# Performance work log

Hardware: AMD Instinct MI355X
Metric: run time of the kernel (lower is better)

Reference implementation:

```python
import jax, jax.numpy as jnp
import numpy as np

D = 512
SEG_LEN = 128
RCL = 32          # right_context_length
K = 31            # depthwise kernel size
STATE = K - 1     # state_size = 30
U = 2048          # utterance length = 16 segments * SEG_LEN
R = 512           # right context length total = 16 * RCL
B = 32
EPS = 1e-5


def layer_norm(x, g, b):
    m = jnp.mean(x, axis=-1, keepdims=True)
    v = jnp.mean((x - m) ** 2, axis=-1, keepdims=True)
    return (x - m) * jax.lax.rsqrt(v + EPS) * g + b


def dwconv(x, w, b):
    # x: [N, D, T], w: [D, 1, K] depthwise, b: [D]
    y = jax.lax.conv_general_dilated(
        x, w, window_strides=(1,), padding='VALID',
        dimension_numbers=('NCH', 'OIH', 'NCH'), feature_group_count=x.shape[1])
    return y + b[None, :, None]


def setup_inputs() -> dict:
    key = jax.random.key(0)
    ks = jax.random.split(key, 8)
    s = 0.02
    return {
        'utterance': jax.random.normal(ks[0], (U, B, D), jnp.float32),
        'right_context': jax.random.normal(ks[1], (R, B, D), jnp.float32),
        'state': jnp.zeros((B, D, STATE), jnp.float32),
        'ln1_g': jnp.ones((D,), jnp.float32),
        'ln1_b': jnp.zeros((D,), jnp.float32),
        'w1': jax.random.normal(ks[2], (2 * D, D), jnp.float32) * s,
        'b1': jnp.zeros((2 * D,), jnp.float32),
        'conv_w': jax.random.normal(ks[3], (D, 1, K), jnp.float32) * s,
        'conv_b': jnp.zeros((D,), jnp.float32),
        'ln2_g': jnp.ones((D,), jnp.float32),
        'ln2_b': jnp.zeros((D,), jnp.float32),
        'w2': jax.random.normal(ks[4], (D, D), jnp.float32) * s,
        'b2': jnp.zeros((D,), jnp.float32),
    }


def reference(utterance, right_context, state, ln1_g, ln1_b, w1, b1,
              conv_w, conv_b, ln2_g, ln2_b, w2, b2):
    inp = jnp.concatenate((right_context, utterance), axis=0)  # [R+U, B, D]
    # pre_conv: LayerNorm -> Linear(D, 2D) -> GLU
    x = layer_norm(inp, ln1_g, ln1_b) @ w1.T + b1
    a, g = jnp.split(x, 2, axis=-1)
    x = a * jax.nn.sigmoid(g)                                  # [R+U, B, D]
    x_rc, x_utt = x[:R], x[R:]
    x_utt_t = jnp.transpose(x_utt, (1, 2, 0))                  # [B, D, U]
    state_x = jnp.concatenate([state, x_utt_t], axis=2)        # [B, D, STATE+U]
    conv_utt = jnp.transpose(dwconv(state_x, conv_w, conv_b), (2, 0, 1))  # [U, B, D]
    # right-context block conv (vectorized segment splicing)
    S = R // RCL
    su = jnp.transpose(state_x, (2, 0, 1))                     # [STATE+U, B, D]
    rc_seg = x_rc.reshape(S, RCL, B, D).transpose(0, 2, 1, 3).reshape(S * B, RCL, D)
    offs = (jnp.arange(S) + 1) * SEG_LEN                       # start = end - STATE
    idx = offs[:, None] + jnp.arange(STATE)[None, :]           # [S, STATE]
    pads = su[idx]                                             # [S, STATE, B, D]
    pads = pads.transpose(0, 2, 1, 3).reshape(S * B, STATE, D)
    block = jnp.transpose(jnp.concatenate([pads, rc_seg], axis=1), (0, 2, 1))  # [S*B, D, STATE+RCL]
    conv_rc = dwconv(block, conv_w, conv_b)                    # [S*B, D, RCL]
    conv_rc = conv_rc.reshape(S, B, D, RCL).transpose(0, 3, 1, 2).reshape(R, B, D)
    y = jnp.concatenate([conv_rc, conv_utt], axis=0)           # [R+U, B, D]
    # post_conv: LayerNorm -> SiLU -> Linear -> (dropout p=0) ; residual add
    out = jax.nn.silu(layer_norm(y, ln2_g, ln2_b)) @ w2.T + b2 + inp
    new_state = state_x[:, :, -STATE:]
    return out[R:], out[:R], new_state
```

## Files before the change

### kernel.cpp

```cpp
#include <hip/hip_runtime.h>


#define Dm 512
#define STATE 30
#define Uu 2048
#define Rr 512
#define Bb 32
#define Tt 2560
#define MROWS 81920

typedef unsigned short u16;
typedef unsigned int u32;
typedef __attribute__((ext_vector_type(8))) __bf16 bf16x8;
typedef __attribute__((ext_vector_type(4))) float f32x4;

__device__ __forceinline__ u16 f2bf(float x) {
  u32 u = __float_as_uint(x);
  u += 0x7fff + ((u >> 16) & 1);
  return (u16)(u >> 16);
}
__device__ __forceinline__ float bf2f(u16 h) {
  return __uint_as_float((u32)h << 16);
}
__device__ __forceinline__ void load_lds16(const void* g, void* l) {
  __builtin_amdgcn_global_load_lds(
      (const __attribute__((address_space(1))) void*)g,
      (__attribute__((address_space(3))) void*)l, 16, 0, 0);
}

__global__ __launch_bounds__(256, 4) void k_cast(const float* __restrict__ src,
                                                 u16* __restrict__ dst, int n) {
  int i = (blockIdx.x * 256 + threadIdx.x) * 4;
  if (i >= n) return;
  float4 v = *(const float4*)(src + i);
  u32 lo = (u32)f2bf(v.x) | ((u32)f2bf(v.y) << 16);
  u32 hi = (u32)f2bf(v.z) | ((u32)f2bf(v.w) << 16);
  *(uint2*)(dst + i) = make_uint2(lo, hi);
}

__global__ __launch_bounds__(256, 4) void k_wt(const float* __restrict__ cw,
                                               float* __restrict__ cwT) {
  int i = blockIdx.x * 256 + threadIdx.x;
  if (i >= 31 * 512) return;
  int k = i >> 9, d = i & 511;
  cwT[i] = cw[d * 31 + k];
}

__global__ __launch_bounds__(256, 4) void k_ln1(const float* __restrict__ utt,
                                                const float* __restrict__ rc,
                                                const float* __restrict__ g,
                                                const float* __restrict__ b,
                                                u16* __restrict__ out) {
  int wid = threadIdx.x >> 6, lane = threadIdx.x & 63;
  long row = (long)blockIdx.x * 4 + wid;
  const float* src = (row < (long)Rr * Bb) ? rc + row * Dm
                                           : utt + (row - (long)Rr * Bb) * Dm;
  int d0 = lane * 8;
  float4 v0 = *(const float4*)(src + d0);
  float4 v1 = *(const float4*)(src + d0 + 4);
  float s = v0.x + v0.y + v0.z + v0.w + v1.x + v1.y + v1.z + v1.w;
  float ss = v0.x * v0.x + v0.y * v0.y + v0.z * v0.z + v0.w * v0.w +
             v1.x * v1.x + v1.y * v1.y + v1.z * v1.z + v1.w * v1.w;
#pragma unroll
  for (int off = 1; off < 64; off <<= 1) {
    s += __shfl_xor(s, off);
    ss += __shfl_xor(ss, off);
  }
  float mean = s * (1.f / 512.f);
  float var = ss * (1.f / 512.f) - mean * mean;
  float rstd = rsqrtf(var + 1e-5f);
  float4 g0 = *(const float4*)(g + d0);
  float4 g1 = *(const float4*)(g + d0 + 4);
  float4 b0 = *(const float4*)(b + d0);
  float4 b1v = *(const float4*)(b + d0 + 4);
  float o[8];
  o[0] = (v0.x - mean) * rstd * g0.x + b0.x;
  o[1] = (v0.y - mean) * rstd * g0.y + b0.y;
  o[2] = (v0.z - mean) * rstd * g0.z + b0.z;
  o[3] = (v0.w - mean) * rstd * g0.w + b0.w;
  o[4] = (v1.x - mean) * rstd * g1.x + b1v.x;
  o[5] = (v1.y - mean) * rstd * g1.y + b1v.y;
  o[6] = (v1.z - mean) * rstd * g1.z + b1v.z;
  o[7] = (v1.w - mean) * rstd * g1.w + b1v.w;
  u32 p[4];
#pragma unroll
  for (int i = 0; i < 4; ++i)
    p[i] = (u32)f2bf(o[2 * i]) | ((u32)f2bf(o[2 * i + 1]) << 16);
  *(uint4*)(out + row * Dm + d0) = make_uint4(p[0], p[1], p[2], p[3]);
}

__global__ __launch_bounds__(256, 2) void k_gemm1(const u16* __restrict__ A,
                                                  const u16* __restrict__ Wb,
                                                  const float* __restrict__ b1,
                                                  u16* __restrict__ X) {
  __shared__ __align__(16) u16 sA[128 * 64], sBa[128 * 64], sBg[128 * 64];
  int tid = threadIdx.x;
  int bid = blockIdx.x;
  int bm = bid % 640, nt = bid / 640;
  long arow0 = (long)bm * 128;
  int ncol0 = nt * 128;
  int lane = tid & 63, wid = tid >> 6;
  int wm = (wid >> 1) * 64, wn = (wid & 1) * 64;
  int lr = lane & 15, kg = lane >> 4;

  f32x4 acc_a[4][4], acc_g[4][4];
#pragma unroll
  for (int i = 0; i < 4; ++i)
#pragma unroll
    for (int j = 0; j < 4; ++j) {
      acc_a[i][j] = (f32x4)0.f;
      acc_g[i][j] = (f32x4)0.f;
    }

  for (int k0 = 0; k0 < 512; k0 += 64) {
#pragma unroll
    for (int i = 0; i < 4; ++i) {
      int c = i * 256 + tid;
      int r = c >> 3, col = (c & 7) * 8;
      load_lds16(A + (arow0 + r) * 512 + k0 + col, &sA[c * 8]);
      load_lds16(Wb + (long)(ncol0 + r) * 512 + k0 + col, &sBa[c * 8]);
      load_lds16(Wb + (long)(512 + ncol0 + r) * 512 + k0 + col, &sBg[c * 8]);
    }
    __syncthreads();
#pragma unroll
    for (int kf = 0; kf < 2; ++kf) {
      bf16x8 av[4], bav[4], bgv[4];
#pragma unroll
      for (int i = 0; i < 4; ++i) {
        av[i] = *(const bf16x8*)&sA[(wm + i * 16 + lr) * 64 + kf * 32 + kg * 8];
        bav[i] = *(const bf16x8*)&sBa[(wn + i * 16 + lr) * 64 + kf * 32 + kg * 8];
        bgv[i] = *(const bf16x8*)&sBg[(wn + i * 16 + lr) * 64 + kf * 32 + kg * 8];
      }
#pragma unroll
      for (int mi = 0; mi < 4; ++mi)
#pragma unroll
        for (int ni = 0; ni < 4; ++ni) {
          acc_a[mi][ni] = __builtin_amdgcn_mfma_f32_16x16x32_bf16(
              av[mi], bav[ni], acc_a[mi][ni], 0, 0, 0);
          acc_g[mi][ni] = __builtin_amdgcn_mfma_f32_16x16x32_bf16(
              av[mi], bgv[ni], acc_g[mi][ni], 0, 0, 0);
        }
    }
    __syncthreads();
  }
  int mg = kg * 4;
#pragma unroll
  for (int mi = 0; mi < 4; ++mi) {
#pragma unroll
    for (int ni = 0; ni < 4; ++ni) {
      int ncol = ncol0 + wn + ni * 16 + lr;
      float ba = b1[ncol], bg = b1[512 + ncol];
#pragma unroll
      for (int rgi = 0; rgi < 4; ++rgi) {
        long row = arow0 + wm + mi * 16 + mg + rgi;
        float a = acc_a[mi][ni][rgi] + ba;
        float gg = acc_g[mi][ni][rgi] + bg;
        float val = a / (1.f + __expf(-gg));
        X[row * 512 + ncol] = f2bf(val);
      }
    }
  }
}

__global__ __launch_bounds__(512, 4) void k_conv_ln2(
    const u16* __restrict__ X, const float* __restrict__ state,
    const float* __restrict__ cwT, const float* __restrict__ cb,
    const float* __restrict__ g2, const float* __restrict__ bt2,
    u16* __restrict__ Z) {
  __shared__ float ys[16][512];
  __shared__ float stats[16][2];
  int d = threadIdx.x;
  int tile = blockIdx.x, b = blockIdx.y;

  float w[31];
#pragma unroll
  for (int k = 0; k < 31; ++k) w[k] = cwT[k * 512 + d];
  float cbd = cb[d];
  float acc[16];
#pragma unroll
  for (int r = 0; r < 16; ++r) acc[r] = cbd;

  const u16* Xc = X + (long)b * 512 + d;
  auto xrow = [&](long trow) -> float { return bf2f(Xc[trow * (long)(Bb * Dm)]); };
  auto step = [&](int j, float x) {
#pragma unroll
    for (int r = 0; r < 16; ++r) {
      int k = j - r;
      if (k >= 0 && k < 31) acc[r] += x * w[k];
    }
  };

  if (tile < 128) {
    long t0 = (long)tile * 16;
    if (tile < 2) {
      const float* st = state + ((long)b * 512 + d) * 30;
#pragma unroll
      for (int j = 0; j < 46; ++j) {
        long tj = t0 - 30 + j;
        float x = (tj < 0) ? st[tj + 30] : xrow(Rr + tj);
        step(j, x);
        if ((j & 15) == 15) __builtin_amdgcn_sched_barrier(0);
      }
    } else {
      long r0 = (long)Rr + t0 - 30;
#pragma unroll
      for (int j = 0; j < 46; ++j) {
        step(j, xrow(r0 + j));
        if ((j & 15) == 15) __builtin_amdgcn_sched_barrier(0);
      }
    }
  } else if (tile < 144) {
    int s = tile - 128;
    long rp = (long)Rr + 128 * (s + 1) - 30;
    long rm = (long)32 * s - 30;
#pragma unroll
    for (int j = 0; j < 30; ++j) {
      step(j, xrow(rp + j));
      if ((j & 15) == 15) __builtin_amdgcn_sched_barrier(0);
    }
#pragma unroll
    for (int j = 30; j < 46; ++j) step(j, xrow(rm + j));
  } else {
    int s = tile - 144;
    long rp = (long)Rr + 128 * (s + 1) - 14;
    long rm = (long)32 * s - 14;
#pragma unroll
    for (int j = 0; j < 14; ++j) step(j, xrow(rp + j));
    __builtin_amdgcn_sched_barrier(0);
#pragma unroll
    for (int j = 14; j < 46; ++j) {
      step(j, xrow(rm + j));
      if ((j & 15) == 15) __builtin_amdgcn_sched_barrier(0);
    }
  }

#pragma unroll
  for (int r = 0; r < 16; ++r) ys[r][d] = acc[r];
  __syncthreads();

  int wid = d >> 6, lane = d & 63;
#pragma unroll
  for (int rr = 0; rr < 2; ++rr) {
    int r = wid * 2 + rr;
    float4 va = *(const float4*)&ys[r][lane * 8];
    float4 vb = *(const float4*)&ys[r][lane * 8 + 4];
    float s = va.x + va.y + va.z + va.w + vb.x + vb.y + vb.z + vb.w;
    float ss = va.x * va.x + va.y * va.y + va.z * va.z + va.w * va.w +
               vb.x * vb.x + vb.y * vb.y + vb.z * vb.z + vb.w * vb.w;
#pragma unroll
    for (int off = 1; off < 64; off <<= 1) {
      s += __shfl_xor(s, off);
      ss += __shfl_xor(ss, off);
    }
    if (lane == 0) {
      float mean = s * (1.f / 512.f);
      float var = ss * (1.f / 512.f) - mean * mean;
      stats[r][0] = mean;
      stats[r][1] = rsqrtf(var + 1e-5f);
    }
  }
  __syncthreads();

  float gg = g2[d], bb = bt2[d];
  long orow0;
  if (tile < 128) {
    orow0 = ((long)Rr + tile * 16) * Bb + b;
  } else if (tile < 144) {
    orow0 = (long)(32 * (tile - 128)) * Bb + b;
  } else {
    orow0 = (long)(32 * (tile - 144) + 16) * Bb + b;
  }
#pragma unroll
  for (int r = 0; r < 16; ++r) {
    float mean = stats[r][0], rstd = stats[r][1];
    float y = (acc[r] - mean) * rstd * gg + bb;
    float zz = y / (1.f + __expf(-y));
    Z[(orow0 + (long)r * Bb) * 512 + d] = f2bf(zz);
  }
}

__global__ __launch_bounds__(256, 2) void k_gemm2(const u16* __restrict__ A,
                                                  const u16* __restrict__ Wb,
                                                  const float* __restrict__ b2,
                                                  const float* __restrict__ utt,
                                                  const float* __restrict__ rc,
                                                  float* __restrict__ out) {
  __shared__ __align__(16) u16 sA[128 * 64], sB[128 * 64];
  int tid = threadIdx.x;
  int bid = blockIdx.x;
  int bm = bid % 640, nt = bid / 640;
  long arow0 = (long)bm * 128;
  int ncol0 = nt * 128;
  int lane = tid & 63, wid = tid >> 6;
  int wm = (wid >> 1) * 64, wn = (wid & 1) * 64;
  int lr = lane & 15, kg = lane >> 4;

  f32x4 acc[4][4];
#pragma unroll
  for (int i = 0; i < 4; ++i)
#pragma unroll
    for (int j = 0; j < 4; ++j) acc[i][j] = (f32x4)0.f;

  for (int k0 = 0; k0 < 512; k0 += 64) {
#pragma unroll
    for (int i = 0; i < 4; ++i) {
      int c = i * 256 + tid;
      int r = c >> 3, col = (c & 7) * 8;
      load_lds16(A + (arow0 + r) * 512 + k0 + col, &sA[c * 8]);
      load_lds16(Wb + (long)(ncol0 + r) * 512 + k0 + col, &sB[c * 8]);
    }
    __syncthreads();
#pragma unroll
    for (int kf = 0; kf < 2; ++kf) {
      bf16x8 av[4], bv[4];
#pragma unroll
      for (int i = 0; i < 4; ++i) {
        av[i] = *(const bf16x8*)&sA[(wm + i * 16 + lr) * 64 + kf * 32 + kg * 8];
        bv[i] = *(const bf16x8*)&sB[(wn + i * 16 + lr) * 64 + kf * 32 + kg * 8];
      }
#pragma unroll
      for (int mi = 0; mi < 4; ++mi)
#pragma unroll
        for (int ni = 0; ni < 4; ++ni)
          acc[mi][ni] = __builtin_amdgcn_mfma_f32_16x16x32_bf16(
              av[mi], bv[ni], acc[mi][ni], 0, 0, 0);
    }
    __syncthreads();
  }
  int mg = kg * 4;
#pragma unroll
  for (int mi = 0; mi < 4; ++mi) {
#pragma unroll
    for (int ni = 0; ni < 4; ++ni) {
      int ncol = ncol0 + wn + ni * 16 + lr;
      float bv = b2[ncol];
#pragma unroll
      for (int rgi = 0; rgi < 4; ++rgi) {
        long row = arow0 + wm + mi * 16 + mg + rgi;
        float val = acc[mi][ni][rgi] + bv;
        const float* src = (row < 16384) ? rc + row * 512 : utt + (row - 16384) * 512;
        val += src[ncol];
        float* dst = (row < 16384) ? out + 33554432 + row * 512
                                   : out + (row - 16384) * 512;
        dst[ncol] = val;
      }
    }
  }
}

__global__ __launch_bounds__(256, 4) void k_state(const u16* __restrict__ X,
                                                  float* __restrict__ out) {
  int i = blockIdx.x * 256 + threadIdx.x;
  if (i >= 491520) return;
  int j = i % 30;
  int rest = i / 30;
  int d = rest & 511;
  int b = rest >> 9;
  out[41943040 + i] = bf2f(X[((long)(2530 + j) * Bb + b) * 512 + d]);
}

extern "C" void kernel_launch(void* const* d_in, const int* in_sizes, int n_in,
                              void* d_out, int out_size, void* d_ws, size_t ws_size,
                              hipStream_t stream) {
  const float* utt = (const float*)d_in[0];
  const float* rc = (const float*)d_in[1];
  const float* state = (const float*)d_in[2];
  const float* ln1g = (const float*)d_in[3];
  const float* ln1b = (const float*)d_in[4];
  const float* w1 = (const float*)d_in[5];
  const float* b1 = (const float*)d_in[6];
  const float* cw = (const float*)d_in[7];
  const float* cb = (const float*)d_in[8];
  const float* ln2g = (const float*)d_in[9];
  const float* ln2b = (const float*)d_in[10];
  const float* w2 = (const float*)d_in[11];
  const float* b2 = (const float*)d_in[12];
  float* out = (float*)d_out;

  char* ws = (char*)d_ws;
  u16* w1b = (u16*)ws;
  u16* w2b = (u16*)(ws + (1 << 20));
  float* cwT = (float*)(ws + (1 << 20) + (1 << 19));
  u16* lnx = (u16*)(ws + (1 << 20) + (1 << 19) + (1 << 16));
  u16* xbuf = lnx + (size_t)MROWS * Dm;

  k_cast<<<512, 256, 0, stream>>>(w1, w1b, 1024 * 512);
  k_cast<<<256, 256, 0, stream>>>(w2, w2b, 512 * 512);
  k_wt<<<62, 256, 0, stream>>>(cw, cwT);
  k_ln1<<<MROWS / 4, 256, 0, stream>>>(utt, rc, ln1g, ln1b, lnx);
  k_gemm1<<<2560, 256, 0, stream>>>(lnx, w1b, b1, xbuf);
  k_conv_ln2<<<dim3(160, 32), 512, 0, stream>>>(xbuf, state, cwT, cb, ln2g, ln2b, lnx);
  k_gemm2<<<2560, 256, 0, stream>>>(lnx, w2b, b2, utt, rc, out);
  k_state<<<1920, 256, 0, stream>>>(xbuf, out);
}
```

Before: 388.8 us.

## Double-buffer LDS K-tiles in both GEMM kernels to overlap loads with MFMA

Both GEMM kernels switch from a single 64-wide K tile in shared memory to two 32-wide K buffers that alternate. The next tile is issued into the spare buffer before the MFMA work on the current one, so global-to-LDS traffic can overlap compute, and each step needs one barrier instead of two. Total LDS use stays the same, but the loop now runs twice as many shorter iterations. The narrower 64-byte LDS row stride may change bank-conflict behaviour on the fragment reads.

```diff
diff --git a/kernel.cpp b/kernel.cpp
--- a/kernel.cpp
+++ b/kernel.cpp
@@ -93,7 +93,7 @@
                                                   const u16* __restrict__ Wb,
                                                   const float* __restrict__ b1,
                                                   u16* __restrict__ X) {
-  __shared__ __align__(16) u16 sA[128 * 64], sBa[128 * 64], sBg[128 * 64];
+  __shared__ __align__(16) u16 sA[2][128 * 32], sBa[2][128 * 32], sBg[2][128 * 32];
   int tid = threadIdx.x;
   int bid = blockIdx.x;
   int bm = bid % 640, nt = bid / 640;
@@ -112,35 +112,38 @@
       acc_g[i][j] = (f32x4)0.f;
     }
 
-  for (int k0 = 0; k0 < 512; k0 += 64) {
+  auto STAGE = [&](int buf, int k0) {
+#pragma unroll
+    for (int i = 0; i < 2; ++i) {
+      int c = i * 256 + tid;
+      int r = c >> 2, col = (c & 3) * 8;
+      load_lds16(A + (arow0 + r) * 512 + k0 + col, &sA[buf][c * 8]);
+      load_lds16(Wb + (long)(ncol0 + r) * 512 + k0 + col, &sBa[buf][c * 8]);
+      load_lds16(Wb + (long)(512 + ncol0 + r) * 512 + k0 + col, &sBg[buf][c * 8]);
+    }
+  };
+
+  STAGE(0, 0);
+  __syncthreads();
+  for (int it = 0; it < 16; ++it) {
+    int cur = it & 1;
+    if (it < 15) STAGE(cur ^ 1, (it + 1) * 32);
+    bf16x8 av[4], bav[4], bgv[4];
 #pragma unroll
     for (int i = 0; i < 4; ++i) {
-      int c = i * 256 + tid;
-      int r = c >> 3, col = (c & 7) * 8;
-      load_lds16(A + (arow0 + r) * 512 + k0 + col, &sA[c * 8]);
-      load_lds16(Wb + (long)(ncol0 + r) * 512 + k0 + col, &sBa[c * 8]);
-      load_lds16(Wb + (long)(512 + ncol0 + r) * 512 + k0 + col, &sBg[c * 8]);
-    }
-    __syncthreads();
-#pragma unroll
-    for (int kf = 0; kf < 2; ++kf) {
-      bf16x8 av[4], bav[4], bgv[4];
-#pragma unroll
-      for (int i = 0; i < 4; ++i) {
-        av[i] = *(const bf16x8*)&sA[(wm + i * 16 + lr) * 64 + kf * 32 + kg * 8];
-        bav[i] = *(const bf16x8*)&sBa[(wn + i * 16 + lr) * 64 + kf * 32 + kg * 8];
-        bgv[i] = *(const bf16x8*)&sBg[(wn + i * 16 + lr) * 64 + kf * 32 + kg * 8];
+      av[i] = *(const bf16x8*)&sA[cur][(wm + i * 16 + lr) * 32 + kg * 8];
+      bav[i] = *(const bf16x8*)&sBa[cur][(wn + i * 16 + lr) * 32 + kg * 8];
+      bgv[i] = *(const bf16x8*)&sBg[cur][(wn + i * 16 + lr) * 32 + kg * 8];
+    }
+#pragma unroll
+    for (int mi = 0; mi < 4; ++mi)
+#pragma unroll
+      for (int ni = 0; ni < 4; ++ni) {
+        acc_a[mi][ni] = __builtin_amdgcn_mfma_f32_16x16x32_bf16(
+            av[mi], bav[ni], acc_a[mi][ni], 0, 0, 0);
+        acc_g[mi][ni] = __builtin_amdgcn_mfma_f32_16x16x32_bf16(
+            av[mi], bgv[ni], acc_g[mi][ni], 0, 0, 0);
       }
-#pragma unroll
-      for (int mi = 0; mi < 4; ++mi)
-#pragma unroll
-        for (int ni = 0; ni < 4; ++ni) {
-          acc_a[mi][ni] = __builtin_amdgcn_mfma_f32_16x16x32_bf16(
-              av[mi], bav[ni], acc_a[mi][ni], 0, 0, 0);
-          acc_g[mi][ni] = __builtin_amdgcn_mfma_f32_16x16x32_bf16(
-              av[mi], bgv[ni], acc_g[mi][ni], 0, 0, 0);
-        }
-    }
     __syncthreads();
   }
   int mg = kg * 4;
@@ -285,7 +288,7 @@
                                                   const float* __restrict__ utt,
                                                   const float* __restrict__ rc,
                                                   float* __restrict__ out) {
-  __shared__ __align__(16) u16 sA[128 * 64], sB[128 * 64];
+  __shared__ __align__(16) u16 sA[2][128 * 32], sB[2][128 * 32];
   int tid = threadIdx.x;
   int bid = blockIdx.x;
   int bm = bid % 640, nt = bid / 640;
@@ -301,30 +304,33 @@
 #pragma unroll
     for (int j = 0; j < 4; ++j) acc[i][j] = (f32x4)0.f;
 
-  for (int k0 = 0; k0 < 512; k0 += 64) {
+  auto STAGE = [&](int buf, int k0) {
+#pragma unroll
+    for (int i = 0; i < 2; ++i) {
+      int c = i * 256 + tid;
+      int r = c >> 2, col = (c & 3) * 8;
+      load_lds16(A + (arow0 + r) * 512 + k0 + col, &sA[buf][c * 8]);
+      load_lds16(Wb + (long)(ncol0 + r) * 512 + k0 + col, &sB[buf][c * 8]);
+    }
+  };
+
+  STAGE(0, 0);
+  __syncthreads();
+  for (int it = 0; it < 16; ++it) {
+    int cur = it & 1;
+    if (it < 15) STAGE(cur ^ 1, (it + 1) * 32);
+    bf16x8 av[4], bv[4];
 #pragma unroll
     for (int i = 0; i < 4; ++i) {
-      int c = i * 256 + tid;
-      int r = c >> 3, col = (c & 7) * 8;
-      load_lds16(A + (arow0 + r) * 512 + k0 + col, &sA[c * 8]);
-      load_lds16(Wb + (long)(ncol0 + r) * 512 + k0 + col, &sB[c * 8]);
-    }
-    __syncthreads();
-#pragma unroll
-    for (int kf = 0; kf < 2; ++kf) {
-      bf16x8 av[4], bv[4];
-#pragma unroll
-      for (int i = 0; i < 4; ++i) {
-        av[i] = *(const bf16x8*)&sA[(wm + i * 16 + lr) * 64 + kf * 32 + kg * 8];
-        bv[i] = *(const bf16x8*)&sB[(wn + i * 16 + lr) * 64 + kf * 32 + kg * 8];
-      }
-#pragma unroll
-      for (int mi = 0; mi < 4; ++mi)
-#pragma unroll
-        for (int ni = 0; ni < 4; ++ni)
-          acc[mi][ni] = __builtin_amdgcn_mfma_f32_16x16x32_bf16(
-              av[mi], bv[ni], acc[mi][ni], 0, 0, 0);
-    }
+      av[i] = *(const bf16x8*)&sA[cur][(wm + i * 16 + lr) * 32 + kg * 8];
+      bv[i] = *(const bf16x8*)&sB[cur][(wn + i * 16 + lr) * 32 + kg * 8];
+    }
+#pragma unroll
+    for (int mi = 0; mi < 4; ++mi)
+#pragma unroll
+      for (int ni = 0; ni < 4; ++ni)
+        acc[mi][ni] = __builtin_amdgcn_mfma_f32_16x16x32_bf16(
+            av[mi], bv[ni], acc[mi][ni], 0, 0, 0);
     __syncthreads();
   }
   int mg = kg * 4;
```

Result: slower. 430.3 us (+10.7%).

## Stage conv input rows in LDS and reorder GEMM block tile mapping

Applied to the files above, without the earlier changes.

In the conv+LayerNorm kernel, each block now loads its 46 input rows into shared memory with 16-byte wide loads, then runs the depthwise conv from LDS. Before, every thread did strided 2-byte global loads. Both GEMM kernels now map neighbouring block IDs to the four N tiles of the same M tile, so a given A tile is reused from L2 by consecutive blocks. The conv kernel's occupancy hint drops from 4 to 2 blocks per SM, and it gains an extra barrier.

```diff
diff --git a/kernel.cpp b/kernel.cpp
--- a/kernel.cpp
+++ b/kernel.cpp
@@ -96,7 +96,7 @@
   __shared__ __align__(16) u16 sA[128 * 64], sBa[128 * 64], sBg[128 * 64];
   int tid = threadIdx.x;
   int bid = blockIdx.x;
-  int bm = bid % 640, nt = bid / 640;
+  int bm = bid >> 2, nt = bid & 3;
   long arow0 = (long)bm * 128;
   int ncol0 = nt * 128;
   int lane = tid & 63, wid = tid >> 6;
@@ -162,15 +162,18 @@
   }
 }
 
-__global__ __launch_bounds__(512, 4) void k_conv_ln2(
+__global__ __launch_bounds__(512, 2) void k_conv_ln2(
     const u16* __restrict__ X, const float* __restrict__ state,
     const float* __restrict__ cwT, const float* __restrict__ cb,
     const float* __restrict__ g2, const float* __restrict__ bt2,
     u16* __restrict__ Z) {
-  __shared__ float ys[16][512];
+  __shared__ __align__(16) u16 stX[46 * 512];
   __shared__ float stats[16][2];
+  float* ys = (float*)stX;
+
   int d = threadIdx.x;
   int tile = blockIdx.x, b = blockIdx.y;
+  int wv = d >> 6, ln = d & 63;
 
   float w[31];
 #pragma unroll
@@ -180,8 +183,6 @@
 #pragma unroll
   for (int r = 0; r < 16; ++r) acc[r] = cbd;
 
-  const u16* Xc = X + (long)b * 512 + d;
-  auto xrow = [&](long trow) -> float { return bf2f(Xc[trow * (long)(Bb * Dm)]); };
   auto step = [&](int j, float x) {
 #pragma unroll
     for (int r = 0; r < 16; ++r) {
@@ -190,60 +191,59 @@
     }
   };
 
-  if (tile < 128) {
+  const u16* Xb = X + (long)b * 512;
+
+  if (tile >= 2) {
+    if (tile < 128) {
+      long base = (long)Rr + tile * 16 - 30;
+      for (int r = wv; r < 46; r += 8)
+        load_lds16(Xb + (base + r) * 16384 + ln * 8, &stX[r * 512 + ln * 8]);
+    } else if (tile < 144) {
+      int s = tile - 128;
+      for (int r = wv; r < 46; r += 8) {
+        long trow = (r < 30) ? ((long)Rr + 128 * (s + 1) - 30 + r)
+                             : ((long)32 * s + r - 30);
+        load_lds16(Xb + trow * 16384 + ln * 8, &stX[r * 512 + ln * 8]);
+      }
+    } else {
+      int s = tile - 144;
+      for (int r = wv; r < 46; r += 8) {
+        long trow = (r < 14) ? ((long)Rr + 128 * (s + 1) - 14 + r)
+                             : ((long)32 * s + r - 14);
+        load_lds16(Xb + trow * 16384 + ln * 8, &stX[r * 512 + ln * 8]);
+      }
+    }
+    __syncthreads();
+#pragma unroll
+    for (int j = 0; j < 46; ++j) {
+      float x = bf2f(stX[j * 512 + d]);
+      step(j, x);
+      if ((j & 7) == 7) __builtin_amdgcn_sched_barrier(0);
+    }
+  } else {
     long t0 = (long)tile * 16;
-    if (tile < 2) {
-      const float* st = state + ((long)b * 512 + d) * 30;
-#pragma unroll
-      for (int j = 0; j < 46; ++j) {
-        long tj = t0 - 30 + j;
-        float x = (tj < 0) ? st[tj + 30] : xrow(Rr + tj);
-        step(j, x);
-        if ((j & 15) == 15) __builtin_amdgcn_sched_barrier(0);
-      }
-    } else {
-      long r0 = (long)Rr + t0 - 30;
-#pragma unroll
-      for (int j = 0; j < 46; ++j) {
-        step(j, xrow(r0 + j));
-        if ((j & 15) == 15) __builtin_amdgcn_sched_barrier(0);
-      }
-    }
-  } else if (tile < 144) {
-    int s = tile - 128;
-    long rp = (long)Rr + 128 * (s + 1) - 30;
-    long rm = (long)32 * s - 30;
-#pragma unroll
-    for (int j = 0; j < 30; ++j) {
-      step(j, xrow(rp + j));
+    const float* st = state + ((long)b * 512 + d) * 30;
+    const u16* Xc = X + (long)b * 512 + d;
+#pragma unroll
+    for (int j = 0; j < 46; ++j) {
+      long tj = t0 - 30 + j;
+      float x = (tj < 0) ? st[tj + 30]
+                         : bf2f(Xc[((long)Rr + tj) * 16384]);
+      step(j, x);
       if ((j & 15) == 15) __builtin_amdgcn_sched_barrier(0);
     }
-#pragma unroll
-    for (int j = 30; j < 46; ++j) step(j, xrow(rm + j));
-  } else {
-    int s = tile - 144;
-    long rp = (long)Rr + 128 * (s + 1) - 14;
-    long rm = (long)32 * s - 14;
-#pragma unroll
-    for (int j = 0; j < 14; ++j) step(j, xrow(rp + j));
-    __builtin_amdgcn_sched_barrier(0);
-#pragma unroll
-    for (int j = 14; j < 46; ++j) {
-      step(j, xrow(rm + j));
-      if ((j & 15) == 15) __builtin_amdgcn_sched_barrier(0);
-    }
-  }
-
-#pragma unroll
-  for (int r = 0; r < 16; ++r) ys[r][d] = acc[r];
+  }
+
   __syncthreads();
-
-  int wid = d >> 6, lane = d & 63;
+#pragma unroll
+  for (int r = 0; r < 16; ++r) ys[r * 512 + d] = acc[r];
+  __syncthreads();
+
 #pragma unroll
   for (int rr = 0; rr < 2; ++rr) {
-    int r = wid * 2 + rr;
-    float4 va = *(const float4*)&ys[r][lane * 8];
-    float4 vb = *(const float4*)&ys[r][lane * 8 + 4];
+    int r = wv * 2 + rr;
+    float4 va = *(const float4*)&ys[r * 512 + ln * 8];
+    float4 vb = *(const float4*)&ys[r * 512 + ln * 8 + 4];
     float s = va.x + va.y + va.z + va.w + vb.x + vb.y + vb.z + vb.w;
     float ss = va.x * va.x + va.y * va.y + va.z * va.z + va.w * va.w +
                vb.x * vb.x + vb.y * vb.y + vb.z * vb.z + vb.w * vb.w;
@@ -252,7 +252,7 @@
       s += __shfl_xor(s, off);
       ss += __shfl_xor(ss, off);
     }
-    if (lane == 0) {
+    if (ln == 0) {
       float mean = s * (1.f / 512.f);
       float var = ss * (1.f / 512.f) - mean * mean;
       stats[r][0] = mean;
@@ -288,7 +288,7 @@
   __shared__ __align__(16) u16 sA[128 * 64], sB[128 * 64];
   int tid = threadIdx.x;
   int bid = blockIdx.x;
-  int bm = bid % 640, nt = bid / 640;
+  int bm = bid >> 2, nt = bid & 3;
   long arow0 = (long)bm * 128;
   int ncol0 = nt * 128;
   int lane = tid & 63, wid = tid >> 6;
```

After: 380.2 us. 1.02x faster.
